# Performance work log

Measured on AMD Instinct MI355X. Metric: run time of the kernel, lower is better.

Reference implementation:

```python
import jax, jax.numpy as jnp
import numpy as np
import math

NUM_SEGMENTS = 4      # num_bezier_segments
SHARPNESS = 75.0
SAMPLE_RATE = 16      # curve samples per bezier segment


def _control_radians(S):
    # replicates the __init__ control-polygon angle construction
    theta = math.pi * 2 / (4 * S) + math.atan(math.tan(2 * math.pi / (4 * S)) / 3.0)
    r = []
    for i in range(S):
        base = 2 * math.pi / S * i
        r += [base, base + theta, 2 * math.pi / S * (i + 1) - theta]
    return jnp.asarray(np.asarray(r, dtype=np.float32).reshape(S, 3))


def _quat_rotate_inv(q, p):
    # rotate p (...,3) by the conjugate of quaternion q (...,4), wxyz convention
    q = q / jnp.linalg.norm(q, axis=-1, keepdims=True)
    w = q[..., 0:1]
    v = -q[..., 1:4]
    t = 2.0 * jnp.cross(v, p)
    return p + w * t + jnp.cross(v, t)


def _csg_stump(points, primitive_parameters, iw, uw, is_training):
    pp = jnp.swapaxes(primitive_parameters, 1, 2)          # (B,K,P)
    B, K, P = pp.shape
    S, R = NUM_SEGMENTS, SAMPLE_RATE
    quat = pp[:, :, :4]
    trans = pp[:, :, 4:7]
    height = pp[:, :, 7]                                   # (B,K)
    radius = jnp.abs(pp[:, :, 8:8 + 3 * S].reshape(B, K, S, 3))
    wts = jnp.abs(pp[:, :, 8 + 3 * S:8 + 5 * S].reshape(B, K, S, 2))

    rad = _control_radians(S)                              # (S,3)
    cp = jnp.stack([jnp.cos(rad) * radius, jnp.sin(rad) * radius], axis=-1)  # (B,K,S,3,2)

    # closed rational cubic bezier spline: segment s uses cp[s,0..2] and cp[s+1,0]
    P0, P1, P2 = cp[:, :, :, 0], cp[:, :, :, 1], cp[:, :, :, 2]
    P3 = jnp.roll(P0, -1, axis=2)
    t = jnp.arange(R, dtype=pp.dtype) / R                  # (R,) endpoint-free
    b0 = (1 - t) ** 3; b1 = 3 * t * (1 - t) ** 2; b2 = 3 * t ** 2 * (1 - t); b3 = t ** 3
    w1 = wts[..., 0:1]; w2 = wts[..., 1:2]                 # (B,K,S,1)
    num = (b0[:, None] * P0[..., None, :]
           + (b1[:, None] * w1[..., None]) * P1[..., None, :]
           + (b2[:, None] * w2[..., None]) * P2[..., None, :]
           + b3[:, None] * P3[..., None, :])               # (B,K,S,R,2)
    den = b0 + b1 * w1 + b2 * w2 + b3                       # (B,K,S,R)
    curve = (num / den[..., None]).reshape(B, K, S * R, 2)  # (B,K,N,2)

    # transform query points into each primitive's local frame
    p_loc = _quat_rotate_inv(quat[:, None], points[:, :, None, :] - trans[:, None])  # (B,M,K,3)
    pxy = p_loc[..., :2]
    pz = p_loc[..., 2]

    # point-to-curve distances without materializing the (B,M,K,N,2) diff
    p_sq = jnp.sum(pxy * pxy, axis=-1)                      # (B,M,K)
    c_sq = jnp.sum(curve * curve, axis=-1)                  # (B,K,N)
    dots = jnp.einsum('bmkd,bknd->bmkn', pxy, curve)
    d = jnp.sqrt(jnp.maximum(p_sq[..., None] + c_sq[:, None] - 2.0 * dots, 0.0) + 1e-12)
    ud = jnp.min(d, axis=-1)                                # (B,M,K) unsigned 2D distance
    idx = jnp.argmin(d, axis=-1)
    curve_r = jnp.sqrt(c_sq)                                # (B,K,N)
    r_near = jnp.take_along_axis(jnp.broadcast_to(curve_r[:, None], d.shape),
                                 idx[..., None], axis=-1)[..., 0]
    sign = jax.lax.stop_gradient(jnp.where(jnp.sqrt(p_sq) <= r_near, -1.0, 1.0))
    sdf2d = sign * ud

    # extrusion along z
    dz = jnp.abs(pz) - height[:, None, :]
    primitive_sdf = (jnp.minimum(jnp.maximum(sdf2d, dz), 0.0)
                     + jnp.sqrt(jnp.maximum(sdf2d, 0.0) ** 2 + jnp.maximum(dz, 0.0) ** 2 + 1e-12))
    support_distances = ud

    occ = jax.nn.sigmoid(-primitive_sdf * SHARPNESS)        # (B,M,K)

    # soft intersection: bkc,bmk->bmkc selection
    pre_i = iw[:, None] * occ[..., None] + (1.0 - iw)[:, None]    # (B,M,K,C)
    if is_training:
        w = jax.lax.stop_gradient(jax.nn.softmax(pre_i * -40.0, axis=-2))
        inter = jnp.sum(w * pre_i, axis=-2)                 # (B,M,C)
    else:
        inter = jnp.min(pre_i, axis=-2)

    # soft union
    pre_u = uw[:, None, :] * inter                          # (B,M,C)
    if is_training:
        w = jax.lax.stop_gradient(jax.nn.softmax(pre_u * 40.0, axis=-1))
        occupancies = jnp.sum(w * pre_u, axis=-1)           # (B,M)
    else:
        occupancies = jnp.max(pre_u, axis=-1)

    return occupancies, primitive_sdf, inter, support_distances


def setup_inputs() -> dict:
    key = jax.random.key(0)
    k1, k2, k3, k4 = jax.random.split(key, 4)
    B, M, K, C = 4, 8192, 64, 32
    P = 8 + 5 * NUM_SEGMENTS  # 28
    return {
        'sample_point_coordinates': jax.random.uniform(k1, (B, M, 3), dtype=jnp.float32),
        'primitive_parameters': jax.random.normal(k2, (B, P, K), dtype=jnp.float32),
        'intersection_layer_weights': jax.random.uniform(k3, (B, K, C), dtype=jnp.float32),
        'union_layer_weights': jax.random.uniform(k4, (B, C), dtype=jnp.float32),
        'is_training': 1,
    }


def reference(sample_point_coordinates, primitive_parameters, intersection_layer_weights,
              union_layer_weights, is_training):
    return _csg_stump(sample_point_coordinates, primitive_parameters,
                      intersection_layer_weights, union_layer_weights, bool(is_training))
```

## Files before the change

kernel.cpp:

```cpp
#include <hip/hip_runtime.h>
#include <math.h>

#define Bb 4
#define Mm 8192
#define Kk 64
#define Cc 32
#define Pp 28

#define OFF_PSDF  (Bb*Mm)
#define OFF_INTER (Bb*Mm + Bb*Mm*Kk)
#define OFF_SD    (Bb*Mm + Bb*Mm*Kk + Bb*Mm*Cc)

#define W40    57.707801635558535f
#define NL2_40 (-0.017328679513998632f)
#define S75    108.20212806667225f
#define EPS_OCC 1e-6f

#define OCC_STRIDE 36
#define TBL_OFF    2304

struct Rad12 { float v[12]; };

__device__ __forceinline__ float fexp2(float x){ return __builtin_amdgcn_exp2f(x); }
__device__ __forceinline__ float frcp(float x){ return __builtin_amdgcn_rcpf(x); }

__global__ __launch_bounds__(256)
void curve_prep(const float* __restrict__ pp, const float* __restrict__ iw_g,
                Rad12 rad,
                float* __restrict__ ws_c, float* __restrict__ params_ws,
                float2* __restrict__ st_ws)
{
    const int g = blockIdx.x * 256 + threadIdx.x;
    const int k = g & 63;
    const int n = (g >> 6) & 63;
    const int b = g >> 12;

#define PP(p) pp[((b * Pp) + (p)) * Kk + k]

    const int s  = n >> 4;
    const int it = n & 15;
    const float t = (float)it * 0.0625f;
    const int s1 = (s + 1) & 3;

    float r0 = fabsf(PP(8 + 3 * s + 0));
    float r1 = fabsf(PP(8 + 3 * s + 1));
    float r2 = fabsf(PP(8 + 3 * s + 2));
    float r3 = fabsf(PP(8 + 3 * s1 + 0));
    float w1 = fabsf(PP(20 + 2 * s + 0));
    float w2 = fabsf(PP(20 + 2 * s + 1));

    float a0 = rad.v[3 * s + 0], a1 = rad.v[3 * s + 1];
    float a2 = rad.v[3 * s + 2], a3 = rad.v[3 * s1 + 0];

    float P0x = cosf(a0) * r0, P0y = sinf(a0) * r0;
    float P1x = cosf(a1) * r1, P1y = sinf(a1) * r1;
    float P2x = cosf(a2) * r2, P2y = sinf(a2) * r2;
    float P3x = cosf(a3) * r3, P3y = sinf(a3) * r3;

    float omt = 1.0f - t;
    float b0 = omt * omt * omt;
    float b1 = (3.0f * t) * (omt * omt);
    float b2 = (3.0f * (t * t)) * omt;
    float b3 = t * t * t;
    float bw1 = b1 * w1, bw2 = b2 * w2;
    float den = ((b0 + bw1) + bw2) + b3;
    float nx  = ((b0 * P0x + bw1 * P1x) + bw2 * P2x) + b3 * P3x;
    float ny  = ((b0 * P0y + bw1 * P1y) + bw2 * P2y) + b3 * P3y;

    float cx = nx / den, cy = ny / den;
    const int j = n >> 1, h = n & 1;
    float* base = ws_c + (((b * 32 + j) * 64) + k) * 4;
    base[h]     = -2.0f * cx;
    base[2 + h] = -2.0f * cy;

    if (n < 8) {
        float val;
        if (n < 4) {
            float q0 = PP(0), q1 = PP(1), q2 = PP(2), q3 = PP(3);
            float nrm = sqrtf(q0 * q0 + q1 * q1 + q2 * q2 + q3 * q3);
            val = PP(n) / nrm;
        } else {
            val = PP(n);
        }
        params_ws[(b * Kk + k) * 8 + n] = val;
    }
#undef PP

    if (blockIdx.x == 0 && threadIdx.x < 128) {
        const int tb = threadIdx.x >> 5, tc = threadIdx.x & 31;
        float S = 0.0f, T = 0.0f;
        for (int kk = 0; kk < 64; ++kk) {
            float w   = iw_g[tb * 2048 + kk * 32 + tc];
            float b40 = (w - 1.0f) * W40;
            float e   = fexp2(b40);
            S += e;
            T  = fmaf(e, b40, T);
        }
        st_ws[threadIdx.x] = make_float2(S, T);
    }
}

__global__ __launch_bounds__(512)
void csg_main(const float* __restrict__ pts, const float* __restrict__ iw_g,
              const float* __restrict__ uw_g, const int* __restrict__ flag,
              const float* __restrict__ ws_c, const float* __restrict__ params_ws,
              const float2* __restrict__ st_ws, float* __restrict__ out)
{
    __shared__ __align__(16) float s_pool[8192];

    const int tid = threadIdx.x;
    const int bid = blockIdx.x;
    const int b   = bid >> 8;
    const int m0  = (bid & 255) << 5;

    float wreg[4];
    {
        const float4* cs = (const float4*)(ws_c + (size_t)b * 8192);
        float4* cd = (float4*)s_pool;
#pragma unroll
        for (int i = 0; i < 4; ++i) cd[tid + i * 512] = cs[tid + i * 512];
#pragma unroll
        for (int i = 0; i < 4; ++i) wreg[i] = iw_g[b * 2048 + tid + i * 512];
    }
    __syncthreads();

    const int wid  = tid >> 6;
    const int lane = tid & 63;
    const int k    = lane;
    const int pt0  = b * Mm + m0 + (wid << 2);

    const float4* prm4 = (const float4*)(params_ws + ((b << 6) + k) * 8);
    float4 q4 = prm4[0];
    float4 t4 = prm4[1];

    const float4* pts4 = (const float4*)(pts + (size_t)pt0 * 3);
    float4 A = pts4[0], Bv = pts4[1], Cv = pts4[2];
    float pxs[4] = {A.x, A.w, Bv.z, Cv.y};
    float pys[4] = {A.y, Bv.x, Bv.w, Cv.z};
    float pzs[4] = {A.z, Bv.y, Cv.x, Cv.w};

    float px4[4], py4[4], plzv[4], psq[4];
    {
        float vx = -q4.y, vy = -q4.z, vz = -q4.w, qw = q4.x;
#pragma unroll
        for (int p = 0; p < 4; ++p) {
            float px = pxs[p] - t4.x, py = pys[p] - t4.y, pz = pzs[p] - t4.z;
            float t1x = 2.0f * (vy * pz - vz * py);
            float t1y = 2.0f * (vz * px - vx * pz);
            float t1z = 2.0f * (vx * py - vy * px);
            float plx = px + qw * t1x + (vy * t1z - vz * t1y);
            float ply = py + qw * t1y + (vz * t1x - vx * t1z);
            plzv[p] = pz + qw * t1z + (vx * t1y - vy * t1x);
            psq[p]  = plx * plx + ply * ply;
            px4[p]  = 4.0f * plx;
            py4[p]  = 4.0f * ply;
        }
    }

    float best4[4] = {1e30f, 1e30f, 1e30f, 1e30f};
    float bcsq4[4] = {0.0f, 0.0f, 0.0f, 0.0f};
    {
        const float4* cdp = (const float4*)&s_pool[k * 4];
#pragma unroll 4
        for (int j = 0; j < 32; ++j) {
            float4 cd = cdp[j * 64];
            float cq4x = fmaf(cd.x, cd.x, cd.z * cd.z);
            float cq4y = fmaf(cd.y, cd.y, cd.w * cd.w);
#pragma unroll
            for (int p = 0; p < 4; ++p) {
                float da = fmaf(cd.x, px4[p], fmaf(cd.z, py4[p], cq4x));
                if (da < best4[p]) { best4[p] = da; bcsq4[p] = cq4x; }
                float db = fmaf(cd.y, px4[p], fmaf(cd.w, py4[p], cq4y));
                if (db < best4[p]) { best4[p] = db; bcsq4[p] = cq4y; }
            }
        }
    }

    float occ[4];
    unsigned long long mu = 0ull;
#pragma unroll
    for (int p = 0; p < 4; ++p) {
        float d2    = psq[p] + 0.25f * best4[p];
        float bq    = 0.25f * bcsq4[p];
        float ud    = sqrtf(fmaxf(d2, 0.0f) + 1e-12f);
        float sgn   = (psq[p] <= bq) ? -1.0f : 1.0f;
        float sdf2d = sgn * ud;
        float dzv   = fabsf(plzv[p]) - t4.w;
        float inner = fminf(fmaxf(sdf2d, dzv), 0.0f);
        float r1m   = fmaxf(sdf2d, 0.0f), r2m = fmaxf(dzv, 0.0f);
        float psdf  = inner + sqrtf(r1m * r1m + r2m * r2m + 1e-12f);
        out[OFF_PSDF + (pt0 + p) * Kk + k] = psdf;
        out[OFF_SD   + (pt0 + p) * Kk + k] = ud;
        occ[p]  = frcp(1.0f + fexp2(S75 * psdf));
        mu |= __ballot(occ[p] > EPS_OCC);
    }

    const int c  = lane & 31;
    const int hi = lane >> 5;
    float2 s0t0 = st_ws[b * 32 + c];

    __syncthreads();
    {
        *(float4*)&s_pool[k * OCC_STRIDE + (wid << 2)] =
            make_float4(occ[0], occ[1], occ[2], occ[3]);
#pragma unroll
        for (int i = 0; i < 4; ++i) {
            int idx = tid + i * 512;
            float w = wreg[i];
            ((float2*)&s_pool[TBL_OFF])[idx] = make_float2(w * (-W40), (w - 1.0f) * W40);
        }
    }
    __syncthreads();

    const int training = flag[0];
    const float2* tbl = (const float2*)&s_pool[TBL_OFF];
    const int ows = wid << 2;
    const int kb  = hi << 5;

    float inter[4];
    if (training) {
        float sw[4], swp[4];
#pragma unroll
        for (int p = 0; p < 4; ++p) {
            sw[p]  = hi ? 0.0f : s0t0.x;
            swp[p] = hi ? 0.0f : s0t0.y;
        }
        unsigned long long m = hi ? (mu >> 32) : (mu & 0xFFFFFFFFull);
        while (m) {
            int kk = __builtin_ctzll(m) + kb; m &= m - 1;
            float4 o4 = *(const float4*)&s_pool[kk * OCC_STRIDE + ows];
            float2 wv = tbl[kk * 32 + c];
            float e0  = fexp2(wv.y);
            float e0b = e0 * wv.y;
            float os[4] = {o4.x, o4.y, o4.z, o4.w};
#pragma unroll
            for (int p = 0; p < 4; ++p) {
                float pre = fmaf(wv.x, os[p], wv.y);
                float e   = fexp2(pre);
                sw[p]  += (e - e0);
                swp[p] += fmaf(e, pre, -e0b);
            }
        }
#pragma unroll
        for (int p = 0; p < 4; ++p) {
            float swt  = sw[p]  + __shfl_xor(sw[p], 32, 64);
            float swpt = swp[p] + __shfl_xor(swp[p], 32, 64);
            inter[p] = swpt * frcp(swt) * NL2_40;
        }
    } else {
        float mx[4] = {-1e30f, -1e30f, -1e30f, -1e30f};
#pragma unroll 8
        for (int j = 0; j < 32; ++j) {
            int kk = kb + j;
            float4 o4 = *(const float4*)&s_pool[kk * OCC_STRIDE + ows];
            float2 wv = tbl[kk * 32 + c];
            float os[4] = {o4.x, o4.y, o4.z, o4.w};
#pragma unroll
            for (int p = 0; p < 4; ++p)
                mx[p] = fmaxf(mx[p], fmaf(wv.x, os[p], wv.y));
        }
#pragma unroll
        for (int p = 0; p < 4; ++p) {
            float m2 = fmaxf(mx[p], __shfl_xor(mx[p], 32, 64));
            inter[p] = m2 * NL2_40;
        }
    }

    if (lane < Cc) {
#pragma unroll
        for (int p = 0; p < 4; ++p)
            out[OFF_INTER + (pt0 + p) * Cc + c] = inter[p];
    }

    float uwv = uw_g[b * Cc + c];
    float resv[4];
    if (training) {
#pragma unroll
        for (int p = 0; p < 4; ++p) {
            float pu  = uwv * inter[p];
            float e   = fexp2(W40 * pu);
            float num = e * pu, den = e;
#pragma unroll
            for (int msk = 16; msk >= 1; msk >>= 1) {
                num += __shfl_xor(num, msk, 64);
                den += __shfl_xor(den, msk, 64);
            }
            resv[p] = num * frcp(den);
        }
    } else {
#pragma unroll
        for (int p = 0; p < 4; ++p) {
            float pu = uwv * inter[p];
#pragma unroll
            for (int msk = 16; msk >= 1; msk >>= 1)
                pu = fmaxf(pu, __shfl_xor(pu, msk, 64));
            resv[p] = pu;
        }
    }
    if (lane == 0)
        *(float4*)(out + pt0) = make_float4(resv[0], resv[1], resv[2], resv[3]);
}

extern "C" void kernel_launch(void* const* d_in, const int* in_sizes, int n_in,
                              void* d_out, int out_size, void* d_ws, size_t ws_size,
                              hipStream_t stream)
{
    const float* pts  = (const float*)d_in[0];
    const float* pp   = (const float*)d_in[1];
    const float* iw   = (const float*)d_in[2];
    const float* uw   = (const float*)d_in[3];
    const int*   flag = (const int*)d_in[4];
    float* out = (float*)d_out;

    float*  ws_c   = (float*)d_ws;
    float*  params = ws_c + 32768;
    float2* st_ws  = (float2*)(params + 2048);

    Rad12 rad;
    const double th = M_PI * 2.0 / 16.0 + atan(tan(2.0 * M_PI / 16.0) / 3.0);
    for (int i = 0; i < 4; ++i) {
        double base = 2.0 * M_PI / 4.0 * (double)i;
        rad.v[3 * i + 0] = (float)base;
        rad.v[3 * i + 1] = (float)(base + th);
        rad.v[3 * i + 2] = (float)(2.0 * M_PI / 4.0 * (double)(i + 1) - th);
    }

    curve_prep<<<64, 256, 0, stream>>>(pp, iw, rad, ws_c, params, st_ws);
    csg_main<<<Bb * Mm / 32, 512, 0, stream>>>(pts, iw, uw, flag,
                                               ws_c, params, st_ws, out);
}
```

Measured before the change: 39.93 us.

## Precompute intersection weight table in prep kernel and exchange occupancies via ds_bpermute

Moves the per-block construction of the intersection-weight exp table (a, b, exp2(b), exp2(b)*b) into the prep kernel, which writes it to a global workspace. The main kernel reads that table directly from global/L2 instead of staging it in shared memory. Occupancies are exchanged within a wavefront with ds_bpermute, so the shared-memory staging and its two block-wide barriers are gone. This removes an exp per iteration and the barriers, but adds global loads of float4 table entries inside the sparse loop and four cross-lane permutes per k.

```diff
diff --git a/kernel.cpp b/kernel.cpp
--- a/kernel.cpp
+++ b/kernel.cpp
@@ -16,19 +16,19 @@
 #define S75    108.20212806667225f
 #define EPS_OCC 1e-6f
 
-#define OCC_STRIDE 36
-#define TBL_OFF    2304
-
 struct Rad12 { float v[12]; };
 
 __device__ __forceinline__ float fexp2(float x){ return __builtin_amdgcn_exp2f(x); }
 __device__ __forceinline__ float frcp(float x){ return __builtin_amdgcn_rcpf(x); }
+__device__ __forceinline__ float bperm(int idx4, float v){
+    return __int_as_float(__builtin_amdgcn_ds_bpermute(idx4, __float_as_int(v)));
+}
 
 __global__ __launch_bounds__(256)
 void curve_prep(const float* __restrict__ pp, const float* __restrict__ iw_g,
                 Rad12 rad,
                 float* __restrict__ ws_c, float* __restrict__ params_ws,
-                float2* __restrict__ st_ws)
+                float2* __restrict__ st_ws, float4* __restrict__ tbl_ws)
 {
     const int g = blockIdx.x * 256 + threadIdx.x;
     const int k = g & 63;
@@ -86,6 +86,15 @@
     }
 #undef PP
 
+    if (n >= 32) {
+        const int idx = (n - 32) * 64 + k;
+        float w  = iw_g[b * 2048 + idx];
+        float a  = w * (-W40);
+        float bb = (w - 1.0f) * W40;
+        float e0 = fexp2(bb);
+        tbl_ws[b * 2048 + idx] = make_float4(a, bb, e0, e0 * bb);
+    }
+
     if (blockIdx.x == 0 && threadIdx.x < 128) {
         const int tb = threadIdx.x >> 5, tc = threadIdx.x & 31;
         float S = 0.0f, T = 0.0f;
@@ -101,10 +110,11 @@
 }
 
 __global__ __launch_bounds__(512)
-void csg_main(const float* __restrict__ pts, const float* __restrict__ iw_g,
-              const float* __restrict__ uw_g, const int* __restrict__ flag,
+void csg_main(const float* __restrict__ pts, const float* __restrict__ uw_g,
+              const int* __restrict__ flag,
               const float* __restrict__ ws_c, const float* __restrict__ params_ws,
-              const float2* __restrict__ st_ws, float* __restrict__ out)
+              const float2* __restrict__ st_ws, const float4* __restrict__ tbl_ws,
+              float* __restrict__ out)
 {
     __shared__ __align__(16) float s_pool[8192];
 
@@ -113,14 +123,11 @@
     const int b   = bid >> 8;
     const int m0  = (bid & 255) << 5;
 
-    float wreg[4];
     {
         const float4* cs = (const float4*)(ws_c + (size_t)b * 8192);
         float4* cd = (float4*)s_pool;
 #pragma unroll
         for (int i = 0; i < 4; ++i) cd[tid + i * 512] = cs[tid + i * 512];
-#pragma unroll
-        for (int i = 0; i < 4; ++i) wreg[i] = iw_g[b * 2048 + tid + i * 512];
     }
     __syncthreads();
 
@@ -197,25 +204,11 @@
 
     const int c  = lane & 31;
     const int hi = lane >> 5;
+    const int kb = hi << 5;
     float2 s0t0 = st_ws[b * 32 + c];
-
-    __syncthreads();
-    {
-        *(float4*)&s_pool[k * OCC_STRIDE + (wid << 2)] =
-            make_float4(occ[0], occ[1], occ[2], occ[3]);
-#pragma unroll
-        for (int i = 0; i < 4; ++i) {
-            int idx = tid + i * 512;
-            float w = wreg[i];
-            ((float2*)&s_pool[TBL_OFF])[idx] = make_float2(w * (-W40), (w - 1.0f) * W40);
-        }
-    }
-    __syncthreads();
+    const float4* tbl4 = tbl_ws + b * 2048;
 
     const int training = flag[0];
-    const float2* tbl = (const float2*)&s_pool[TBL_OFF];
-    const int ows = wid << 2;
-    const int kb  = hi << 5;
 
     float inter[4];
     if (training) {
@@ -228,17 +221,19 @@
         unsigned long long m = hi ? (mu >> 32) : (mu & 0xFFFFFFFFull);
         while (m) {
             int kk = __builtin_ctzll(m) + kb; m &= m - 1;
-            float4 o4 = *(const float4*)&s_pool[kk * OCC_STRIDE + ows];
-            float2 wv = tbl[kk * 32 + c];
-            float e0  = fexp2(wv.y);
-            float e0b = e0 * wv.y;
-            float os[4] = {o4.x, o4.y, o4.z, o4.w};
+            int i4 = kk << 2;
+            float o0 = bperm(i4, occ[0]);
+            float o1 = bperm(i4, occ[1]);
+            float o2 = bperm(i4, occ[2]);
+            float o3 = bperm(i4, occ[3]);
+            float4 wv = tbl4[kk * 32 + c];
+            float os[4] = {o0, o1, o2, o3};
 #pragma unroll
             for (int p = 0; p < 4; ++p) {
                 float pre = fmaf(wv.x, os[p], wv.y);
                 float e   = fexp2(pre);
-                sw[p]  += (e - e0);
-                swp[p] += fmaf(e, pre, -e0b);
+                sw[p]  += (e - wv.z);
+                swp[p] += fmaf(e, pre, -wv.w);
             }
         }
 #pragma unroll
@@ -249,12 +244,13 @@
         }
     } else {
         float mx[4] = {-1e30f, -1e30f, -1e30f, -1e30f};
-#pragma unroll 8
+#pragma unroll 4
         for (int j = 0; j < 32; ++j) {
             int kk = kb + j;
-            float4 o4 = *(const float4*)&s_pool[kk * OCC_STRIDE + ows];
-            float2 wv = tbl[kk * 32 + c];
-            float os[4] = {o4.x, o4.y, o4.z, o4.w};
+            int i4 = kk << 2;
+            float4 wv = tbl4[kk * 32 + c];
+            float os[4] = {bperm(i4, occ[0]), bperm(i4, occ[1]),
+                           bperm(i4, occ[2]), bperm(i4, occ[3])};
 #pragma unroll
             for (int p = 0; p < 4; ++p)
                 mx[p] = fmaxf(mx[p], fmaf(wv.x, os[p], wv.y));
@@ -315,6 +311,7 @@
     float*  ws_c   = (float*)d_ws;
     float*  params = ws_c + 32768;
     float2* st_ws  = (float2*)(params + 2048);
+    float4* tbl_ws = (float4*)((char*)d_ws + 140 * 1024);
 
     Rad12 rad;
     const double th = M_PI * 2.0 / 16.0 + atan(tan(2.0 * M_PI / 16.0) / 3.0);
@@ -325,7 +322,7 @@
         rad.v[3 * i + 2] = (float)(2.0 * M_PI / 4.0 * (double)(i + 1) - th);
     }
 
-    curve_prep<<<64, 256, 0, stream>>>(pp, iw, rad, ws_c, params, st_ws);
-    csg_main<<<Bb * Mm / 32, 512, 0, stream>>>(pts, iw, uw, flag,
-                                               ws_c, params, st_ws, out);
+    curve_prep<<<64, 256, 0, stream>>>(pp, iw, rad, ws_c, params, st_ws, tbl_ws);
+    csg_main<<<Bb * Mm / 32, 512, 0, stream>>>(pts, uw, flag,
+                                               ws_c, params, st_ws, tbl_ws, out);
 }
```

Result: no change. 39.68 us (-0.6%).
